# Kernel tuning notes

Hardware: AMD Instinct MI355X
Metric: run time of the kernel (lower is better)

## Reference

```python
import jax, jax.numpy as jnp
import numpy as np

NUM_HEADS = 8
HEAD_DIM = 64
GROUPS = 32
EPS = 1e-5


def setup_inputs() -> dict:
    key = jax.random.key(0)
    ks = jax.random.split(key, 7)
    B, C, H, W = 8, 512, 32, 32
    x = jax.random.normal(ks[0], (B, C, H, W), dtype=jnp.float32)
    gn_w = jnp.ones((C,), dtype=jnp.float32)
    gn_b = jnp.zeros((C,), dtype=jnp.float32)
    # 1x1 convs stored as [out, in] matrices
    qkv_w = jax.random.normal(ks[1], (3 * C, C), dtype=jnp.float32) * (1.0 / np.sqrt(C))
    qkv_b = jnp.zeros((3 * C,), dtype=jnp.float32)
    proj_w = jax.random.normal(ks[2], (C, C), dtype=jnp.float32) * (1.0 / np.sqrt(C))
    proj_b = jnp.zeros((C,), dtype=jnp.float32)
    return {"x": x, "gn_w": gn_w, "gn_b": gn_b, "qkv_w": qkv_w,
            "qkv_b": qkv_b, "proj_w": proj_w, "proj_b": proj_b}


def _group_norm(x, w, b):
    B, C, H, W = x.shape
    xg = x.reshape(B, GROUPS, C // GROUPS, H, W)
    mu = xg.mean(axis=(2, 3, 4), keepdims=True)
    var = xg.var(axis=(2, 3, 4), keepdims=True)
    xn = ((xg - mu) * jax.lax.rsqrt(var + EPS)).reshape(B, C, H, W)
    return xn * w[None, :, None, None] + b[None, :, None, None]


def reference(x, gn_w, gn_b, qkv_w, qkv_b, proj_w, proj_b):
    B, C, H, W = x.shape
    N = H * W
    h = _group_norm(x, gn_w, gn_b)
    # 1x1 conv == per-pixel matmul: [B, 3C, N]
    hf = h.reshape(B, C, N)
    qkv = jnp.einsum('oc,bcn->bon', qkv_w, hf) + qkv_b[None, :, None]
    qkv = qkv.reshape(B, 3, NUM_HEADS, HEAD_DIM, N)
    q, k, v = qkv[:, 0], qkv[:, 1], qkv[:, 2]  # each [B, h, d, N]
    attn = jnp.einsum('bhdi,bhdj->bhij', q, k) * (HEAD_DIM ** -0.5)
    attn = jax.nn.softmax(attn, axis=-1)
    out = jnp.einsum('bhij,bhdj->bhdi', attn, v)  # [B, h, d, N]
    out = out.reshape(B, C, N)
    out = jnp.einsum('oc,bcn->bon', proj_w, out) + proj_b[None, :, None]
    return x + out.reshape(B, C, H, W)
```

## Files before the change

kernel.cpp:

```cpp
#include <hip/hip_runtime.h>
#include <hip/hip_bf16.h>

#define BF16 __hip_bfloat16

typedef __attribute__((ext_vector_type(8))) short bf16x8;
typedef __attribute__((ext_vector_type(4))) float f32x4;
typedef __attribute__((ext_vector_type(4))) unsigned short ushort4v;
typedef __attribute__((ext_vector_type(4))) float float4v;

#define LOG2E 1.44269504089f

__device__ __forceinline__ unsigned short f2bf(float f) {
  BF16 h = __float2bfloat16(f);
  union { BF16 h; unsigned short u; } cv;
  cv.h = h;
  return cv.u;
}

__device__ __forceinline__ void gload_lds16(const BF16* g, BF16* s) {
  __builtin_amdgcn_global_load_lds(
      (const __attribute__((address_space(1))) void*)g,
      (__attribute__((address_space(3))) void*)s, 16, 0, 0);
}

__global__ __launch_bounds__(256) void stats_cast_kernel(const float* __restrict__ x,
                                                         const float* __restrict__ gw,
                                                         const float* __restrict__ gb,
                                                         const float* __restrict__ qw,
                                                         const float* __restrict__ pw,
                                                         float2* __restrict__ stats,
                                                         BF16* __restrict__ wq,
                                                         BF16* __restrict__ wp) {
  const int L = blockIdx.x;
  if (L < 256) {
    const int bb = L & 7, g = L >> 3;
    const float* xg = x + (size_t)(bb * 512 + g * 16) * 1024;
    float s = 0.f, ss = 0.f;
    const float4v* x4 = (const float4v*)xg;
    for (int i = threadIdx.x; i < 4096; i += 256) {
      float4v v = x4[i];
      s  += v[0] + v[1] + v[2] + v[3];
      ss += v[0] * v[0] + v[1] * v[1] + v[2] * v[2] + v[3] * v[3];
    }
    for (int off = 32; off > 0; off >>= 1) {
      s  += __shfl_down(s, off, 64);
      ss += __shfl_down(ss, off, 64);
    }
    __shared__ float sred[8];
    const int wv = threadIdx.x >> 6;
    if ((threadIdx.x & 63) == 0) { sred[wv] = s; sred[4 + wv] = ss; }
    __syncthreads();
    const float S  = sred[0] + sred[1] + sred[2] + sred[3];
    const float SS = sred[4] + sred[5] + sred[6] + sred[7];
    const float mean = S * (1.f / 16384.f);
    const float var  = SS * (1.f / 16384.f) - mean * mean;
    const float rstd = rsqrtf(var + 1e-5f);
    if (threadIdx.x < 16) {
      const int c = g * 16 + threadIdx.x;
      const float aw = gw[c] * rstd;
      float2 st; st.x = aw; st.y = gb[c] - mean * aw;
      stats[bb * 512 + c] = st;
    }
  } else {
    const int i4 = (L - 256) * 256 + threadIdx.x;
    if (i4 < 196608) {
      float4v v = ((const float4v*)qw)[i4];
      ushort4v pk;
      #pragma unroll
      for (int r = 0; r < 4; ++r) pk[r] = f2bf(v[r]);
      *(ushort4v*)&wq[i4 * 4] = pk;
    } else {
      const int j = i4 - 196608;
      float4v v = ((const float4v*)pw)[j];
      ushort4v pk;
      #pragma unroll
      for (int r = 0; r < 4; ++r) pk[r] = f2bf(v[r]);
      *(ushort4v*)&wp[j * 4] = pk;
    }
  }
}

__global__ __launch_bounds__(256) void gn_apply_kernel(const float* __restrict__ x,
                                                       const float2* __restrict__ stats,
                                                       BF16* __restrict__ h_t) {
  const int L = blockIdx.x;
  const int b = L & 7, pxt = L >> 3;
  const int t = threadIdx.x;
  __shared__ __align__(16) BF16 Lt[128 * 8 * 4];

  for (int ct = 0; ct < 4; ++ct) {
    if (ct) __syncthreads();
    #pragma unroll
    for (int k = 0; k < 4; ++k) {
      const int i = k * 256 + t;
      const int ch_l = i >> 3, f4l = i & 7;
      const int cg = ct * 128 + ch_l;
      const float2 st = stats[b * 512 + cg];
      const float4v v =
          ((const float4v*)x)[((size_t)(b * 512 + cg)) * 256 + pxt * 8 + f4l];
      ushort4v pk;
      #pragma unroll
      for (int r = 0; r < 4; ++r) pk[r] = f2bf(v[r] * st.x + st.y);
      const int s = f4l ^ (ch_l & 7) ^ ((ch_l >> 3) & 7);
      *(ushort4v*)&Lt[(ch_l * 8 + s) * 4] = pk;
    }
    __syncthreads();
    #pragma unroll
    for (int rr = 0; rr < 2; ++rr) {
      const int px_l = (rr * 256 + t) >> 4;
      const int c16 = t & 15;
      union { unsigned short u[8]; bf16x8 v8; } o;
      #pragma unroll
      for (int cc = 0; cc < 8; ++cc) {
        const int ch = c16 * 8 + cc;
        const int s = (px_l >> 2) ^ (ch & 7) ^ ((ch >> 3) & 7);
        o.u[cc] = *(const unsigned short*)&Lt[(ch * 8 + s) * 4 + (px_l & 3)];
      }
      *(bf16x8*)&h_t[((size_t)(b * 1024 + pxt * 32 + px_l)) * 512 + ct * 128 +
                     c16 * 8] = o.v8;
    }
  }
}

#define GEMM_CORE(A, B, Al, Bl)                                                \
  const int tid = threadIdx.x, l = tid & 63, wv = tid >> 6;                    \
  const int wm = wv >> 1, wn = wv & 1;                                         \
  const int lc = l & 15, lh = l >> 4;                                          \
  f32x4 acc[4][4] = {};                                                        \
  int srow[4], scg[4];                                                         \
  _Pragma("unroll")                                                            \
  for (int t = 0; t < 4; ++t) {                                                \
    int cidx = t * 256 + wv * 64 + l;                                          \
    srow[t] = cidx >> 3;                                                       \
    scg[t]  = (cidx & 7) ^ (srow[t] & 7);                                      \
  }                                                                            \
  for (int kt = 0; kt < 8; ++kt) {                                             \
    const int k0 = kt * 64;                                                    \
    __syncthreads();                                                           \
    _Pragma("unroll")                                                          \
    for (int t = 0; t < 4; ++t) {                                              \
      gload_lds16(&A[(size_t)srow[t] * 512 + k0 + scg[t] * 8],                 \
                  &Al[(t * 256 + wv * 64) * 8]);                               \
      gload_lds16(&B[(size_t)srow[t] * 512 + k0 + scg[t] * 8],                 \
                  &Bl[(t * 256 + wv * 64) * 8]);                               \
    }                                                                          \
    __syncthreads();                                                           \
    _Pragma("unroll")                                                          \
    for (int ks = 0; ks < 2; ++ks) {                                           \
      bf16x8 af[4], bfr[4];                                                    \
      _Pragma("unroll")                                                        \
      for (int i = 0; i < 4; ++i) {                                            \
        int rA = wm * 64 + i * 16 + lc;                                        \
        int cA = (ks * 4 + lh) ^ (rA & 7);                                     \
        af[i] = *(const bf16x8*)&Al[(rA * 8 + cA) * 8];                        \
        int rB = wn * 64 + i * 16 + lc;                                        \
        int cB = (ks * 4 + lh) ^ (rB & 7);                                     \
        bfr[i] = *(const bf16x8*)&Bl[(rB * 8 + cB) * 8];                       \
      }                                                                        \
      _Pragma("unroll")                                                        \
      for (int i = 0; i < 4; ++i)                                              \
        _Pragma("unroll")                                                      \
        for (int j = 0; j < 4; ++j)                                            \
          acc[i][j] = __builtin_amdgcn_mfma_f32_16x16x32_bf16(af[i], bfr[j],   \
                                                              acc[i][j], 0, 0, 0); \
    }                                                                          \
  }

__global__ __launch_bounds__(256) void qkv_gemm_kernel(const BF16* __restrict__ Wq,
                                                       const BF16* __restrict__ Ht,
                                                       const float* __restrict__ bias,
                                                       BF16* __restrict__ q_t,
                                                       BF16* __restrict__ k_t,
                                                       BF16* __restrict__ v_nat) {
  const int L = blockIdx.x;
  const int b = L & 7, w = L >> 3;
  const int mt = w % 12, nt = w / 12;
  const int m0 = mt * 128, n0 = nt * 128;
  const BF16* A = Wq + (size_t)m0 * 512;
  const BF16* B = Ht + (size_t)b * 1024 * 512 + (size_t)n0 * 512;
  __shared__ __align__(16) BF16 smem[16384];
  BF16* Al = smem;
  BF16* Bl = smem + 8192;
  GEMM_CORE(A, B, Al, Bl)

  __syncthreads();
  BF16* Et = smem;
  if (mt < 8) {
    const float scale = (mt < 4) ? 0.125f * LOG2E : 1.0f;
    #pragma unroll
    for (int mi = 0; mi < 4; ++mi) {
      const int d0 = mi * 16 + 4 * lh;
      const int o  = m0 + wm * 64 + d0;
      const int g  = d0 >> 3;
      #pragma unroll
      for (int ni = 0; ni < 4; ++ni) {
        const int pixl = wn * 64 + ni * 16 + lc;
        f32x4 a = acc[mi][ni];
        ushort4v pk;
        #pragma unroll
        for (int r = 0; r < 4; ++r) pk[r] = f2bf((a[r] + bias[o + r]) * scale);
        const int s = g ^ (pixl & 7);
        *(ushort4v*)&Et[((wm * 128 + pixl) * 8 + s) * 8 + (d0 & 7)] = pk;
      }
    }
    __syncthreads();
    BF16* dstb = (mt < 4) ? q_t : k_t;
    const int hb0 = (mt & 3) * 2;
    #pragma unroll
    for (int rr = 0; rr < 8; ++rr) {
      const int rowI = rr * 32 + (tid >> 3);
      const int h2 = rowI >> 7, pixl = rowI & 127;
      const int j = tid & 7;
      bf16x8 v = *(const bf16x8*)&Et[(rowI * 8 + (j ^ (pixl & 7))) * 8];
      *(bf16x8*)&dstb[((size_t)(b * 8 + hb0 + h2) * 1024 + n0 + pixl) * 64 +
                      j * 8] = v;
    }
  } else {
    #pragma unroll
    for (int mi = 0; mi < 4; ++mi) {
      #pragma unroll
      for (int ni = 0; ni < 4; ++ni) {
        const int pixl = wn * 64 + ni * 16 + lc;
        const int gp = pixl >> 3;
        f32x4 a = acc[mi][ni];
        #pragma unroll
        for (int r = 0; r < 4; ++r) {
          const int vr_l = wm * 64 + mi * 16 + 4 * lh + r;
          const int s = gp ^ (vr_l & 15);
          Et[(vr_l * 16 + s) * 8 + (pixl & 7)] =
              __float2bfloat16(a[r] + bias[m0 + vr_l]);
        }
      }
    }
    __syncthreads();
    const int vr0 = m0 - 1024;
    #pragma unroll
    for (int rr = 0; rr < 8; ++rr) {
      const int vr_l = rr * 16 + (tid >> 4);
      const int gp = tid & 15;
      bf16x8 v = *(const bf16x8*)&Et[(vr_l * 16 + (gp ^ (vr_l & 15))) * 8];
      *(bf16x8*)&v_nat[((size_t)(b * 512 + vr0 + vr_l)) * 1024 + n0 + gp * 8] = v;
    }
  }
}

__global__ __launch_bounds__(256) void proj_gemm_kernel(const BF16* __restrict__ Wp,
                                                        const BF16* __restrict__ At,
                                                        const float* __restrict__ bias,
                                                        const float* __restrict__ x,
                                                        float* __restrict__ out) {
  const int L = blockIdx.x;
  const int b = L & 7, w = L >> 3;
  const int mt = w & 3, nt = w >> 2;
  const int m0 = mt * 128, n0 = nt * 128;
  const BF16* A = Wp + (size_t)m0 * 512;
  const BF16* B = At + (size_t)b * 1024 * 512 + (size_t)n0 * 512;
  __shared__ __align__(16) BF16 smem[16384];
  BF16* Al = smem;
  BF16* Bl = smem + 8192;
  GEMM_CORE(A, B, Al, Bl)

  const int r0 = lh * 4;
  #pragma unroll
  for (int mi = 0; mi < 4; ++mi) {
    #pragma unroll
    for (int ni = 0; ni < 4; ++ni) {
      const int n = n0 + wn * 64 + ni * 16 + lc;
      f32x4 a = acc[mi][ni];
      #pragma unroll
      for (int r = 0; r < 4; ++r) {
        const int c = m0 + wm * 64 + mi * 16 + r0 + r;
        const size_t idx = ((size_t)(b * 512 + c)) * 1024 + n;
        out[idx] = x[idx] + bias[c] + a[r];
      }
    }
  }
}

__global__ __launch_bounds__(256) void attn_kernel(const BF16* __restrict__ q_t,
                                                   const BF16* __restrict__ k_t,
                                                   const BF16* __restrict__ v_nat,
                                                   BF16* __restrict__ attout) {
  const int L = blockIdx.x;
  const int xcd = L & 7, w = L >> 3;
  const int b = xcd, hh = w & 7;
  const int bh = b * 8 + hh;
  const int i0 = (w >> 3) * 128;
  const int tid = threadIdx.x, l = tid & 63, wv = tid >> 6;
  const int lc = l & 15, lh = l >> 4;

  __shared__ __align__(16) BF16 Kl[2][64 * 64];
  __shared__ __align__(16) BF16 Vl[2][64 * 64];
  __shared__ __align__(16) BF16 Pl[4][2][16][72];

  bf16x8 aq[2][2];
  #pragma unroll
  for (int cb = 0; cb < 2; ++cb) {
    const BF16* qp = q_t + ((size_t)bh * 1024 + i0 + wv * 32 + cb * 16 + lc) * 64;
    aq[cb][0] = *(const bf16x8*)&qp[lh * 8];
    aq[cb][1] = *(const bf16x8*)&qp[32 + lh * 8];
  }

  f32x4 O[2][4] = {};
  float mr[2] = {-1e30f, -1e30f}, lr[2] = {0.f, 0.f};

  const BF16* kbase = k_t + (size_t)bh * 1024 * 64;
  const BF16* vbase = v_nat + (size_t)bh * 64 * 1024;

  int srow[2], scg[2];
  #pragma unroll
  for (int it = 0; it < 2; ++it) {
    int cidx = it * 256 + wv * 64 + l;
    srow[it] = cidx >> 3;
    scg[it]  = (cidx & 7) ^ (srow[it] & 7);
  }

  #pragma unroll
  for (int it = 0; it < 2; ++it) {
    gload_lds16(&kbase[(size_t)srow[it] * 64 + scg[it] * 8],
                &Kl[0][(it * 256 + wv * 64) * 8]);
    gload_lds16(&vbase[(size_t)srow[it] * 1024 + scg[it] * 8],
                &Vl[0][(it * 256 + wv * 64) * 8]);
  }

  for (int jt = 0; jt < 16; ++jt) {
    const int cur = jt & 1;
    __syncthreads();
    if (jt < 15) {
      const int j1 = (jt + 1) * 64, nxt = cur ^ 1;
      #pragma unroll
      for (int it = 0; it < 2; ++it) {
        gload_lds16(&kbase[(size_t)(j1 + srow[it]) * 64 + scg[it] * 8],
                    &Kl[nxt][(it * 256 + wv * 64) * 8]);
        gload_lds16(&vbase[(size_t)srow[it] * 1024 + j1 + scg[it] * 8],
                    &Vl[nxt][(it * 256 + wv * 64) * 8]);
      }
    }

    f32x4 Sv[2][4];
    __builtin_amdgcn_s_setprio(1);
    #pragma unroll
    for (int jf = 0; jf < 4; ++jf) {
      const int jl = jf * 16 + lc;
      const int c0 = lh ^ (jl & 7), c1 = (4 + lh) ^ (jl & 7);
      bf16x8 ak0 = *(const bf16x8*)&Kl[cur][(jl * 8 + c0) * 8];
      bf16x8 ak1 = *(const bf16x8*)&Kl[cur][(jl * 8 + c1) * 8];
      #pragma unroll
      for (int cb = 0; cb < 2; ++cb) {
        f32x4 s0 = {};
        s0 = __builtin_amdgcn_mfma_f32_16x16x32_bf16(ak0, aq[cb][0], s0, 0, 0, 0);
        Sv[cb][jf] = __builtin_amdgcn_mfma_f32_16x16x32_bf16(ak1, aq[cb][1], s0, 0, 0, 0);
      }
    }
    __builtin_amdgcn_s_setprio(0);

    #pragma unroll
    for (int cb = 0; cb < 2; ++cb) {
      float tmax = Sv[cb][0][0];
      #pragma unroll
      for (int jf = 0; jf < 4; ++jf)
        #pragma unroll
        for (int r = 0; r < 4; ++r) tmax = fmaxf(tmax, Sv[cb][jf][r]);
      tmax = fmaxf(tmax, __shfl_xor(tmax, 16, 64));
      tmax = fmaxf(tmax, __shfl_xor(tmax, 32, 64));
      if (__any(tmax > mr[cb] + 11.52f)) {
        const float mnew = fmaxf(mr[cb], tmax);
        const float sc = exp2f(mr[cb] - mnew);
        mr[cb] = mnew;
        lr[cb] *= sc;
        #pragma unroll
        for (int nf = 0; nf < 4; ++nf)
          #pragma unroll
          for (int r = 0; r < 4; ++r) O[cb][nf][r] *= sc;
      }
      float rs = 0.f;
      #pragma unroll
      for (int jf = 0; jf < 4; ++jf) {
        ushort4v pk;
        #pragma unroll
        for (int r = 0; r < 4; ++r) {
          float p = exp2f(Sv[cb][jf][r] - mr[cb]);
          rs += p;
          pk[r] = f2bf(p);
        }
        *(ushort4v*)&Pl[wv][cb][lc][jf * 16 + 4 * lh] = pk;
      }
      rs += __shfl_xor(rs, 16, 64);
      rs += __shfl_xor(rs, 32, 64);
      lr[cb] += rs;
    }

    bf16x8 bp[2][2];
    #pragma unroll
    for (int cb = 0; cb < 2; ++cb) {
      bp[cb][0] = *(const bf16x8*)&Pl[wv][cb][lc][lh * 8];
      bp[cb][1] = *(const bf16x8*)&Pl[wv][cb][lc][32 + lh * 8];
    }

    __builtin_amdgcn_s_setprio(1);
    #pragma unroll
    for (int nf = 0; nf < 4; ++nf) {
      const int dl = nf * 16 + lc;
      const int c0 = lh ^ (dl & 7), c1 = (4 + lh) ^ (dl & 7);
      bf16x8 av0 = *(const bf16x8*)&Vl[cur][(dl * 8 + c0) * 8];
      bf16x8 av1 = *(const bf16x8*)&Vl[cur][(dl * 8 + c1) * 8];
      #pragma unroll
      for (int cb = 0; cb < 2; ++cb) {
        O[cb][nf] = __builtin_amdgcn_mfma_f32_16x16x32_bf16(av0, bp[cb][0], O[cb][nf], 0, 0, 0);
        O[cb][nf] = __builtin_amdgcn_mfma_f32_16x16x32_bf16(av1, bp[cb][1], O[cb][nf], 0, 0, 0);
      }
    }
    __builtin_amdgcn_s_setprio(0);
  }

  #pragma unroll
  for (int cb = 0; cb < 2; ++cb) {
    const float inv = 1.0f / lr[cb];
    BF16* dst = attout + ((size_t)b * 1024 + i0 + wv * 32 + cb * 16 + lc) * 512 + hh * 64;
    #pragma unroll
    for (int nf = 0; nf < 4; ++nf) {
      ushort4v pk;
      #pragma unroll
      for (int r = 0; r < 4; ++r) pk[r] = f2bf(O[cb][nf][r] * inv);
      *(ushort4v*)&dst[nf * 16 + 4 * lh] = pk;
    }
  }
}

extern "C" void kernel_launch(void* const* d_in, const int* in_sizes, int n_in,
                              void* d_out, int out_size, void* d_ws, size_t ws_size,
                              hipStream_t stream) {
  const float* x      = (const float*)d_in[0];
  const float* gn_w   = (const float*)d_in[1];
  const float* gn_b   = (const float*)d_in[2];
  const float* qkv_w  = (const float*)d_in[3];
  const float* qkv_b  = (const float*)d_in[4];
  const float* proj_w = (const float*)d_in[5];
  const float* proj_b = (const float*)d_in[6];
  float* out = (float*)d_out;

  char* ws = (char*)d_ws;
  BF16* wq     = (BF16*)(ws);
  BF16* wp     = (BF16*)(ws + 1572864);
  BF16* h_t    = (BF16*)(ws + 2097152);
  BF16* q_t    = (BF16*)(ws + 10485760);
  BF16* k_t    = (BF16*)(ws + 18874368);
  BF16* v_nat  = (BF16*)(ws + 27262976);
  float2* stats = (float2*)(ws + 35651584);
  BF16* attout = h_t;

  stats_cast_kernel<<<1280, 256, 0, stream>>>(x, gn_w, gn_b, qkv_w, proj_w,
                                              stats, wq, wp);
  gn_apply_kernel<<<256, 256, 0, stream>>>(x, stats, h_t);
  qkv_gemm_kernel<<<768, 256, 0, stream>>>(wq, h_t, qkv_b, q_t, k_t, v_nat);
  attn_kernel<<<512, 256, 0, stream>>>(q_t, k_t, v_nat, attout);
  proj_gemm_kernel<<<256, 256, 0, stream>>>(wp, attout, proj_b, x, out);
}
```

Baseline: 171.3 us.

## Use single-wave attention blocks that read K/V directly from global memory

The attention kernel moves from 256-thread blocks that share double-buffered K/V tiles in LDS to 64-thread single-wave blocks, with four times as many blocks. Each wave now loads its K and V fragments straight from global memory, which removes the LDS staging, the per-tile __syncthreads and the setprio hints. The aim is to cut LDS footprint and barrier overhead so more blocks fit per CU. The cost is that K/V reuse across waves is lost, so global and L2 traffic grow about fourfold, and the global loads are no longer prefetched ahead of the MFMAs.

```diff
diff --git a/kernel.cpp b/kernel.cpp
--- a/kernel.cpp
+++ b/kernel.cpp
@@ -277,26 +277,25 @@
   }
 }
 
-__global__ __launch_bounds__(256) void attn_kernel(const BF16* __restrict__ q_t,
-                                                   const BF16* __restrict__ k_t,
-                                                   const BF16* __restrict__ v_nat,
-                                                   BF16* __restrict__ attout) {
+__global__ __launch_bounds__(64) void attn_kernel(const BF16* __restrict__ q_t,
+                                                  const BF16* __restrict__ k_t,
+                                                  const BF16* __restrict__ v_nat,
+                                                  BF16* __restrict__ attout) {
   const int L = blockIdx.x;
-  const int xcd = L & 7, w = L >> 3;
-  const int b = xcd, hh = w & 7;
+  const int b = L & 7;
+  const int w = L >> 3;
+  const int hh = w & 7;
+  const int i0 = (w >> 3) * 32;
   const int bh = b * 8 + hh;
-  const int i0 = (w >> 3) * 128;
-  const int tid = threadIdx.x, l = tid & 63, wv = tid >> 6;
+  const int l = threadIdx.x;
   const int lc = l & 15, lh = l >> 4;
 
-  __shared__ __align__(16) BF16 Kl[2][64 * 64];
-  __shared__ __align__(16) BF16 Vl[2][64 * 64];
-  __shared__ __align__(16) BF16 Pl[4][2][16][72];
+  __shared__ __align__(16) BF16 Pl[2][16][72];
 
   bf16x8 aq[2][2];
   #pragma unroll
   for (int cb = 0; cb < 2; ++cb) {
-    const BF16* qp = q_t + ((size_t)bh * 1024 + i0 + wv * 32 + cb * 16 + lc) * 64;
+    const BF16* qp = q_t + ((size_t)bh * 1024 + i0 + cb * 16 + lc) * 64;
     aq[cb][0] = *(const bf16x8*)&qp[lh * 8];
     aq[cb][1] = *(const bf16x8*)&qp[32 + lh * 8];
   }
@@ -307,44 +306,15 @@
   const BF16* kbase = k_t + (size_t)bh * 1024 * 64;
   const BF16* vbase = v_nat + (size_t)bh * 64 * 1024;
 
-  int srow[2], scg[2];
-  #pragma unroll
-  for (int it = 0; it < 2; ++it) {
-    int cidx = it * 256 + wv * 64 + l;
-    srow[it] = cidx >> 3;
-    scg[it]  = (cidx & 7) ^ (srow[it] & 7);
-  }
-
-  #pragma unroll
-  for (int it = 0; it < 2; ++it) {
-    gload_lds16(&kbase[(size_t)srow[it] * 64 + scg[it] * 8],
-                &Kl[0][(it * 256 + wv * 64) * 8]);
-    gload_lds16(&vbase[(size_t)srow[it] * 1024 + scg[it] * 8],
-                &Vl[0][(it * 256 + wv * 64) * 8]);
-  }
-
   for (int jt = 0; jt < 16; ++jt) {
-    const int cur = jt & 1;
-    __syncthreads();
-    if (jt < 15) {
-      const int j1 = (jt + 1) * 64, nxt = cur ^ 1;
-      #pragma unroll
-      for (int it = 0; it < 2; ++it) {
-        gload_lds16(&kbase[(size_t)(j1 + srow[it]) * 64 + scg[it] * 8],
-                    &Kl[nxt][(it * 256 + wv * 64) * 8]);
-        gload_lds16(&vbase[(size_t)srow[it] * 1024 + j1 + scg[it] * 8],
-                    &Vl[nxt][(it * 256 + wv * 64) * 8]);
-      }
-    }
+    const int j0 = jt * 64;
 
     f32x4 Sv[2][4];
-    __builtin_amdgcn_s_setprio(1);
     #pragma unroll
     for (int jf = 0; jf < 4; ++jf) {
-      const int jl = jf * 16 + lc;
-      const int c0 = lh ^ (jl & 7), c1 = (4 + lh) ^ (jl & 7);
-      bf16x8 ak0 = *(const bf16x8*)&Kl[cur][(jl * 8 + c0) * 8];
-      bf16x8 ak1 = *(const bf16x8*)&Kl[cur][(jl * 8 + c1) * 8];
+      const BF16* krow = kbase + ((size_t)(j0 + jf * 16 + lc)) * 64;
+      bf16x8 ak0 = *(const bf16x8*)&krow[lh * 8];
+      bf16x8 ak1 = *(const bf16x8*)&krow[32 + lh * 8];
       #pragma unroll
       for (int cb = 0; cb < 2; ++cb) {
         f32x4 s0 = {};
@@ -352,15 +322,18 @@
         Sv[cb][jf] = __builtin_amdgcn_mfma_f32_16x16x32_bf16(ak1, aq[cb][1], s0, 0, 0, 0);
       }
     }
-    __builtin_amdgcn_s_setprio(0);
 
     #pragma unroll
     for (int cb = 0; cb < 2; ++cb) {
-      float tmax = Sv[cb][0][0];
-      #pragma unroll
-      for (int jf = 0; jf < 4; ++jf)
-        #pragma unroll
-        for (int r = 0; r < 4; ++r) tmax = fmaxf(tmax, Sv[cb][jf][r]);
+      float m0v = fmaxf(fmaxf(Sv[cb][0][0], Sv[cb][0][1]),
+                        fmaxf(Sv[cb][0][2], Sv[cb][0][3]));
+      float m1v = fmaxf(fmaxf(Sv[cb][1][0], Sv[cb][1][1]),
+                        fmaxf(Sv[cb][1][2], Sv[cb][1][3]));
+      float m2v = fmaxf(fmaxf(Sv[cb][2][0], Sv[cb][2][1]),
+                        fmaxf(Sv[cb][2][2], Sv[cb][2][3]));
+      float m3v = fmaxf(fmaxf(Sv[cb][3][0], Sv[cb][3][1]),
+                        fmaxf(Sv[cb][3][2], Sv[cb][3][3]));
+      float tmax = fmaxf(fmaxf(m0v, m1v), fmaxf(m2v, m3v));
       tmax = fmaxf(tmax, __shfl_xor(tmax, 16, 64));
       tmax = fmaxf(tmax, __shfl_xor(tmax, 32, 64));
       if (__any(tmax > mr[cb] + 11.52f)) {
@@ -383,7 +356,7 @@
           rs += p;
           pk[r] = f2bf(p);
         }
-        *(ushort4v*)&Pl[wv][cb][lc][jf * 16 + 4 * lh] = pk;
+        *(ushort4v*)&Pl[cb][lc][jf * 16 + 4 * lh] = pk;
       }
       rs += __shfl_xor(rs, 16, 64);
       rs += __shfl_xor(rs, 32, 64);
@@ -393,30 +366,27 @@
     bf16x8 bp[2][2];
     #pragma unroll
     for (int cb = 0; cb < 2; ++cb) {
-      bp[cb][0] = *(const bf16x8*)&Pl[wv][cb][lc][lh * 8];
-      bp[cb][1] = *(const bf16x8*)&Pl[wv][cb][lc][32 + lh * 8];
-    }
-
-    __builtin_amdgcn_s_setprio(1);
+      bp[cb][0] = *(const bf16x8*)&Pl[cb][lc][lh * 8];
+      bp[cb][1] = *(const bf16x8*)&Pl[cb][lc][32 + lh * 8];
+    }
+
     #pragma unroll
     for (int nf = 0; nf < 4; ++nf) {
-      const int dl = nf * 16 + lc;
-      const int c0 = lh ^ (dl & 7), c1 = (4 + lh) ^ (dl & 7);
-      bf16x8 av0 = *(const bf16x8*)&Vl[cur][(dl * 8 + c0) * 8];
-      bf16x8 av1 = *(const bf16x8*)&Vl[cur][(dl * 8 + c1) * 8];
+      const BF16* vrow = vbase + ((size_t)(nf * 16 + lc)) * 1024 + j0;
+      bf16x8 av0 = *(const bf16x8*)&vrow[lh * 8];
+      bf16x8 av1 = *(const bf16x8*)&vrow[32 + lh * 8];
       #pragma unroll
       for (int cb = 0; cb < 2; ++cb) {
         O[cb][nf] = __builtin_amdgcn_mfma_f32_16x16x32_bf16(av0, bp[cb][0], O[cb][nf], 0, 0, 0);
         O[cb][nf] = __builtin_amdgcn_mfma_f32_16x16x32_bf16(av1, bp[cb][1], O[cb][nf], 0, 0, 0);
       }
     }
-    __builtin_amdgcn_s_setprio(0);
   }
 
   #pragma unroll
   for (int cb = 0; cb < 2; ++cb) {
     const float inv = 1.0f / lr[cb];
-    BF16* dst = attout + ((size_t)b * 1024 + i0 + wv * 32 + cb * 16 + lc) * 512 + hh * 64;
+    BF16* dst = attout + ((size_t)b * 1024 + i0 + cb * 16 + lc) * 512 + hh * 64;
     #pragma unroll
     for (int nf = 0; nf < 4; ++nf) {
       ushort4v pk;
@@ -453,6 +423,6 @@
                                               stats, wq, wp);
   gn_apply_kernel<<<256, 256, 0, stream>>>(x, stats, h_t);
   qkv_gemm_kernel<<<768, 256, 0, stream>>>(wq, h_t, qkv_b, q_t, k_t, v_nat);
-  attn_kernel<<<512, 256, 0, stream>>>(q_t, k_t, v_nat, attout);
+  attn_kernel<<<2048, 64, 0, stream>>>(q_t, k_t, v_nat, attout);
   proj_gemm_kernel<<<256, 256, 0, stream>>>(wp, attout, proj_b, x, out);
 }
```

Measured after the change: 193.4 us. 1.13x slower.

## Halve attention query tile per block and load V directly from global

Applied to the files above, without the earlier changes.

The attention kernel now handles 64 query rows per block (16 per wave) instead of 128, which doubles the grid to 1024 blocks and cuts per-thread accumulator registers. V tiles are no longer staged through LDS. Each wave reads its V fragments straight from global memory every key step, while K stays double-buffered in LDS. This aims to raise occupancy and parallelism and to shrink LDS use, at the cost of reading K/V twice as often overall and issuing uncoalesced, unprefetched global V loads inside the inner loop.

```diff
diff --git a/kernel.cpp b/kernel.cpp
--- a/kernel.cpp
+++ b/kernel.cpp
@@ -282,27 +282,25 @@
                                                    const BF16* __restrict__ v_nat,
                                                    BF16* __restrict__ attout) {
   const int L = blockIdx.x;
-  const int xcd = L & 7, w = L >> 3;
-  const int b = xcd, hh = w & 7;
+  const int b = L & 7, w = L >> 3;
+  const int hh = w & 7;
+  const int i0 = (w >> 3) * 64;
   const int bh = b * 8 + hh;
-  const int i0 = (w >> 3) * 128;
   const int tid = threadIdx.x, l = tid & 63, wv = tid >> 6;
   const int lc = l & 15, lh = l >> 4;
 
   __shared__ __align__(16) BF16 Kl[2][64 * 64];
-  __shared__ __align__(16) BF16 Vl[2][64 * 64];
-  __shared__ __align__(16) BF16 Pl[4][2][16][72];
-
-  bf16x8 aq[2][2];
-  #pragma unroll
-  for (int cb = 0; cb < 2; ++cb) {
-    const BF16* qp = q_t + ((size_t)bh * 1024 + i0 + wv * 32 + cb * 16 + lc) * 64;
-    aq[cb][0] = *(const bf16x8*)&qp[lh * 8];
-    aq[cb][1] = *(const bf16x8*)&qp[32 + lh * 8];
-  }
-
-  f32x4 O[2][4] = {};
-  float mr[2] = {-1e30f, -1e30f}, lr[2] = {0.f, 0.f};
+  __shared__ __align__(16) BF16 Pl[4][16][72];
+
+  bf16x8 aq0, aq1;
+  {
+    const BF16* qp = q_t + ((size_t)bh * 1024 + i0 + wv * 16 + lc) * 64;
+    aq0 = *(const bf16x8*)&qp[lh * 8];
+    aq1 = *(const bf16x8*)&qp[32 + lh * 8];
+  }
+
+  f32x4 O[4] = {};
+  float mr = -1e30f, lr = 0.f;
 
   const BF16* kbase = k_t + (size_t)bh * 1024 * 64;
   const BF16* vbase = v_nat + (size_t)bh * 64 * 1024;
@@ -310,120 +308,103 @@
   int srow[2], scg[2];
   #pragma unroll
   for (int it = 0; it < 2; ++it) {
-    int cidx = it * 256 + wv * 64 + l;
+    int cidx = it * 256 + tid;
     srow[it] = cidx >> 3;
     scg[it]  = (cidx & 7) ^ (srow[it] & 7);
   }
 
   #pragma unroll
-  for (int it = 0; it < 2; ++it) {
+  for (int it = 0; it < 2; ++it)
     gload_lds16(&kbase[(size_t)srow[it] * 64 + scg[it] * 8],
-                &Kl[0][(it * 256 + wv * 64) * 8]);
-    gload_lds16(&vbase[(size_t)srow[it] * 1024 + scg[it] * 8],
-                &Vl[0][(it * 256 + wv * 64) * 8]);
-  }
+                &Kl[0][(it * 256 + tid) * 8]);
 
   for (int jt = 0; jt < 16; ++jt) {
     const int cur = jt & 1;
+    const int j0 = jt * 64;
     __syncthreads();
     if (jt < 15) {
-      const int j1 = (jt + 1) * 64, nxt = cur ^ 1;
-      #pragma unroll
-      for (int it = 0; it < 2; ++it) {
+      const int j1 = j0 + 64, nxt = cur ^ 1;
+      #pragma unroll
+      for (int it = 0; it < 2; ++it)
         gload_lds16(&kbase[(size_t)(j1 + srow[it]) * 64 + scg[it] * 8],
-                    &Kl[nxt][(it * 256 + wv * 64) * 8]);
-        gload_lds16(&vbase[(size_t)srow[it] * 1024 + j1 + scg[it] * 8],
-                    &Vl[nxt][(it * 256 + wv * 64) * 8]);
-      }
-    }
-
-    f32x4 Sv[2][4];
+                    &Kl[nxt][(it * 256 + tid) * 8]);
+    }
+
+    bf16x8 av[4][2];
+    #pragma unroll
+    for (int nf = 0; nf < 4; ++nf) {
+      const BF16* vrow = vbase + ((size_t)(nf * 16 + lc)) * 1024 + j0;
+      av[nf][0] = *(const bf16x8*)&vrow[lh * 8];
+      av[nf][1] = *(const bf16x8*)&vrow[32 + lh * 8];
+    }
+
+    f32x4 Sv[4];
     __builtin_amdgcn_s_setprio(1);
     #pragma unroll
     for (int jf = 0; jf < 4; ++jf) {
       const int jl = jf * 16 + lc;
       const int c0 = lh ^ (jl & 7), c1 = (4 + lh) ^ (jl & 7);
-      bf16x8 ak0 = *(const bf16x8*)&Kl[cur][(jl * 8 + c0) * 8];
-      bf16x8 ak1 = *(const bf16x8*)&Kl[cur][(jl * 8 + c1) * 8];
-      #pragma unroll
-      for (int cb = 0; cb < 2; ++cb) {
-        f32x4 s0 = {};
-        s0 = __builtin_amdgcn_mfma_f32_16x16x32_bf16(ak0, aq[cb][0], s0, 0, 0, 0);
-        Sv[cb][jf] = __builtin_amdgcn_mfma_f32_16x16x32_bf16(ak1, aq[cb][1], s0, 0, 0, 0);
+      bf16x8 ak = *(const bf16x8*)&Kl[cur][(jl * 8 + c0) * 8];
+      f32x4 s0 = {};
+      s0 = __builtin_amdgcn_mfma_f32_16x16x32_bf16(ak, aq0, s0, 0, 0, 0);
+      ak = *(const bf16x8*)&Kl[cur][(jl * 8 + c1) * 8];
+      Sv[jf] = __builtin_amdgcn_mfma_f32_16x16x32_bf16(ak, aq1, s0, 0, 0, 0);
+    }
+    __builtin_amdgcn_s_setprio(0);
+
+    float tmax = Sv[0][0];
+    #pragma unroll
+    for (int jf = 0; jf < 4; ++jf)
+      #pragma unroll
+      for (int r = 0; r < 4; ++r) tmax = fmaxf(tmax, Sv[jf][r]);
+    tmax = fmaxf(tmax, __shfl_xor(tmax, 16, 64));
+    tmax = fmaxf(tmax, __shfl_xor(tmax, 32, 64));
+    if (__any(tmax > mr + 11.52f)) {
+      const float mnew = fmaxf(mr, tmax);
+      const float sc = exp2f(mr - mnew);
+      mr = mnew;
+      lr *= sc;
+      #pragma unroll
+      for (int nf = 0; nf < 4; ++nf)
+        #pragma unroll
+        for (int r = 0; r < 4; ++r) O[nf][r] *= sc;
+    }
+    float rs = 0.f;
+    #pragma unroll
+    for (int jf = 0; jf < 4; ++jf) {
+      ushort4v pk;
+      #pragma unroll
+      for (int r = 0; r < 4; ++r) {
+        float p = exp2f(Sv[jf][r] - mr);
+        rs += p;
+        pk[r] = f2bf(p);
       }
+      *(ushort4v*)&Pl[wv][lc][jf * 16 + 4 * lh] = pk;
+    }
+    rs += __shfl_xor(rs, 16, 64);
+    rs += __shfl_xor(rs, 32, 64);
+    lr += rs;
+
+    const bf16x8 bp0 = *(const bf16x8*)&Pl[wv][lc][lh * 8];
+    const bf16x8 bp1 = *(const bf16x8*)&Pl[wv][lc][32 + lh * 8];
+
+    __builtin_amdgcn_s_setprio(1);
+    #pragma unroll
+    for (int nf = 0; nf < 4; ++nf) {
+      O[nf] = __builtin_amdgcn_mfma_f32_16x16x32_bf16(av[nf][0], bp0, O[nf], 0, 0, 0);
+      O[nf] = __builtin_amdgcn_mfma_f32_16x16x32_bf16(av[nf][1], bp1, O[nf], 0, 0, 0);
     }
     __builtin_amdgcn_s_setprio(0);
-
-    #pragma unroll
-    for (int cb = 0; cb < 2; ++cb) {
-      float tmax = Sv[cb][0][0];
-      #pragma unroll
-      for (int jf = 0; jf < 4; ++jf)
-        #pragma unroll
-        for (int r = 0; r < 4; ++r) tmax = fmaxf(tmax, Sv[cb][jf][r]);
-      tmax = fmaxf(tmax, __shfl_xor(tmax, 16, 64));
-      tmax = fmaxf(tmax, __shfl_xor(tmax, 32, 64));
-      if (__any(tmax > mr[cb] + 11.52f)) {
-        const float mnew = fmaxf(mr[cb], tmax);
-        const float sc = exp2f(mr[cb] - mnew);
-        mr[cb] = mnew;
-        lr[cb] *= sc;
-        #pragma unroll
-        for (int nf = 0; nf < 4; ++nf)
-          #pragma unroll
-          for (int r = 0; r < 4; ++r) O[cb][nf][r] *= sc;
-      }
-      float rs = 0.f;
-      #pragma unroll
-      for (int jf = 0; jf < 4; ++jf) {
-        ushort4v pk;
-        #pragma unroll
-        for (int r = 0; r < 4; ++r) {
-          float p = exp2f(Sv[cb][jf][r] - mr[cb]);
-          rs += p;
-          pk[r] = f2bf(p);
-        }
-        *(ushort4v*)&Pl[wv][cb][lc][jf * 16 + 4 * lh] = pk;
-      }
-      rs += __shfl_xor(rs, 16, 64);
-      rs += __shfl_xor(rs, 32, 64);
-      lr[cb] += rs;
-    }
-
-    bf16x8 bp[2][2];
-    #pragma unroll
-    for (int cb = 0; cb < 2; ++cb) {
-      bp[cb][0] = *(const bf16x8*)&Pl[wv][cb][lc][lh * 8];
-      bp[cb][1] = *(const bf16x8*)&Pl[wv][cb][lc][32 + lh * 8];
-    }
-
-    __builtin_amdgcn_s_setprio(1);
-    #pragma unroll
-    for (int nf = 0; nf < 4; ++nf) {
-      const int dl = nf * 16 + lc;
-      const int c0 = lh ^ (dl & 7), c1 = (4 + lh) ^ (dl & 7);
-      bf16x8 av0 = *(const bf16x8*)&Vl[cur][(dl * 8 + c0) * 8];
-      bf16x8 av1 = *(const bf16x8*)&Vl[cur][(dl * 8 + c1) * 8];
-      #pragma unroll
-      for (int cb = 0; cb < 2; ++cb) {
-        O[cb][nf] = __builtin_amdgcn_mfma_f32_16x16x32_bf16(av0, bp[cb][0], O[cb][nf], 0, 0, 0);
-        O[cb][nf] = __builtin_amdgcn_mfma_f32_16x16x32_bf16(av1, bp[cb][1], O[cb][nf], 0, 0, 0);
-      }
-    }
-    __builtin_amdgcn_s_setprio(0);
-  }
-
+  }
+
+  const float inv = 1.0f / lr;
+  BF16* dst = attout + ((size_t)b * 1024 + i0 + wv * 16 + lc) * 512 + hh * 64;
   #pragma unroll
-  for (int cb = 0; cb < 2; ++cb) {
-    const float inv = 1.0f / lr[cb];
-    BF16* dst = attout + ((size_t)b * 1024 + i0 + wv * 32 + cb * 16 + lc) * 512 + hh * 64;
-    #pragma unroll
-    for (int nf = 0; nf < 4; ++nf) {
-      ushort4v pk;
-      #pragma unroll
-      for (int r = 0; r < 4; ++r) pk[r] = f2bf(O[cb][nf][r] * inv);
-      *(ushort4v*)&dst[nf * 16 + 4 * lh] = pk;
-    }
+  for (int nf = 0; nf < 4; ++nf) {
+    ushort4v pk;
+    #pragma unroll
+    for (int r = 0; r < 4; ++r) pk[r] = f2bf(O[nf][r] * inv);
+    *(ushort4v*)&dst[nf * 16 + 4 * lh] = pk;
   }
 }
 
@@ -453,6 +434,6 @@
                                               stats, wq, wp);
   gn_apply_kernel<<<256, 256, 0, stream>>>(x, stats, h_t);
   qkv_gemm_kernel<<<768, 256, 0, stream>>>(wq, h_t, qkv_b, q_t, k_t, v_nat);
-  attn_kernel<<<512, 256, 0, stream>>>(q_t, k_t, v_nat, attout);
+  attn_kernel<<<1024, 256, 0, stream>>>(q_t, k_t, v_nat, attout);
   proj_gemm_kernel<<<256, 256, 0, stream>>>(wp, attout, proj_b, x, out);
 }
```

Measured after the change: 208.6 us. +21.8%, slower.
